# Kernel tuning notes

Measured on AMD Instinct MI355X. Metric: run time of the kernel, lower is better.

Reference implementation:

```python
import jax, jax.numpy as jnp
import numpy as np

SEED_ID = 1234  # seed_id from init, masked to 32 bits


def _synth_R(k_iter, d_out, d_in, dtype):
    # Seeded pseudo-random base weight: randn(d_out, d_in) / sqrt(d_in)
    s = (SEED_ID ^ int(k_iter)) & 0xFFFFFFFF
    R = jax.random.normal(jax.random.key(s), (d_out, d_in), dtype=dtype)
    return R * np.float32(1.0 / np.sqrt(d_in))


def setup_inputs() -> dict:
    key = jax.random.key(0)
    kx, kv, ku = jax.random.split(key, 3)
    B, S, D, RANK = 32, 4096, 512, 64
    x = jax.random.normal(kx, (B, S, D), dtype=jnp.float32)
    alpha = jnp.float32(1.0)
    U = jnp.zeros((D, RANK), dtype=jnp.float32)
    # match torch init: V ~ N(0,1)/sqrt(rank)
    V = jax.random.normal(kv, (RANK, D), dtype=jnp.float32) * np.float32(1.0 / np.sqrt(RANK))
    bias = jnp.zeros((D,), dtype=jnp.float32)
    return {"x": x, "alpha": alpha, "U": U, "V": V, "bias": bias, "k_iter": 2}


def reference(x, alpha, U, V, bias, k_iter):
    d_out = U.shape[0]
    d_in = V.shape[1]
    dtype = x.dtype
    R = _synth_R(k_iter, d_out, d_in, dtype)                      # [d_out, d_in]
    W = alpha.astype(dtype) * R + (U.astype(dtype) @ V.astype(dtype))  # [d_out, d_in]
    # F.linear: x @ W.T + b
    return jnp.einsum('bsd,od->bso', x, W) + bias.astype(dtype)
```

## Files before the change

### kernel.cpp

```cpp
#include <hip/hip_runtime.h>
#include <stdint.h>


#define M_TOTAL 131072
#define N_DIM 512
#define K_DIM 512
#define RANK 64

typedef __attribute__((ext_vector_type(8))) short bf16x8;
typedef __attribute__((ext_vector_type(4))) float f32x4;

__device__ __forceinline__ void threefry2x32(uint32_t k0, uint32_t k1,
                                             uint32_t x0, uint32_t x1,
                                             uint32_t& y0, uint32_t& y1) {
  uint32_t ks0 = k0, ks1 = k1, ks2 = k0 ^ k1 ^ 0x1BD11BDAu;
  const uint32_t ks[3] = {ks0, ks1, ks2};
  const int R0[4] = {13, 15, 26, 6};
  const int R1[4] = {17, 29, 16, 24};
  x0 += ks[0];
  x1 += ks[1];
#pragma unroll
  for (int g = 0; g < 5; ++g) {
    const int* r = (g & 1) ? R1 : R0;
#pragma unroll
    for (int i = 0; i < 4; ++i) {
      x0 += x1;
      x1 = (x1 << r[i]) | (x1 >> (32 - r[i]));
      x1 ^= x0;
    }
    x0 += ks[(g + 1) % 3];
    x1 += ks[(g + 2) % 3] + (uint32_t)(g + 1);
  }
  y0 = x0;
  y1 = x1;
}

__device__ __forceinline__ float erfinv_f32(float x) {
  float w = -log1pf(-x * x);
  float p;
  if (w < 5.0f) {
    w = w - 2.5f;
    p = 2.81022636e-08f;
    p = fmaf(p, w, 3.43273939e-07f);
    p = fmaf(p, w, -3.5233877e-06f);
    p = fmaf(p, w, -4.39150654e-06f);
    p = fmaf(p, w, 0.00021858087f);
    p = fmaf(p, w, -0.00125372503f);
    p = fmaf(p, w, -0.00417768164f);
    p = fmaf(p, w, 0.246640727f);
    p = fmaf(p, w, 1.50140941f);
  } else {
    w = sqrtf(w) - 3.0f;
    p = -0.000200214257f;
    p = fmaf(p, w, 0.000100950558f);
    p = fmaf(p, w, 0.00134934322f);
    p = fmaf(p, w, -0.00367342844f);
    p = fmaf(p, w, 0.00573950773f);
    p = fmaf(p, w, -0.0076224613f);
    p = fmaf(p, w, 0.00943887047f);
    p = fmaf(p, w, 1.00167406f);
    p = fmaf(p, w, 2.83297682f);
  }
  return p * x;
}

__device__ __forceinline__ unsigned short f32_to_bf16_rtne(float f) {
  uint32_t x = __float_as_uint(f);
  uint32_t r = (x + 0x7FFFu + ((x >> 16) & 1u)) >> 16;
  return (unsigned short)r;
}

__global__ __launch_bounds__(256) void build_w_kernel(
    const float* __restrict__ alpha_p, const float* __restrict__ U,
    const float* __restrict__ V, const int* __restrict__ k_iter_p,
    unsigned short* __restrict__ Wb) {
  int idx = blockIdx.x * blockDim.x + threadIdx.x;
  uint32_t s = (1234u ^ (uint32_t)(*k_iter_p));
  uint32_t y0, y1;
  threefry2x32(0u, s, 0u, (uint32_t)idx, y0, y1);
  uint32_t bits = y0 ^ y1;
  float u01 = __uint_as_float((bits >> 9) | 0x3f800000u) - 1.0f;
  const float lo = -0.99999994f;
  float u = fmaxf(lo, u01 * 2.0f + lo);
  float rnorm = 1.41421354f * erfinv_f32(u);
  const float scale = 0.044194173824159216f;

  int o = idx >> 9;
  int i = idx & 511;
  float uv = 0.0f;
#pragma unroll 8
  for (int r = 0; r < RANK; ++r)
    uv = fmaf(U[o * RANK + r], V[r * N_DIM + i], uv);

  float w = (*alpha_p) * (rnorm * scale) + uv;
  Wb[idx] = f32_to_bf16_rtne(w);
}

#define BM 128
#define BN 128
#define BK 64
#define LDK 72

__global__ __launch_bounds__(256, 2) void gemm_kernel(
    const float* __restrict__ X, const unsigned short* __restrict__ Wb,
    const float* __restrict__ bias, float* __restrict__ Out) {
  __shared__ unsigned short As[BM][LDK];
  __shared__ unsigned short Bs[BN][LDK];

  const int tid = threadIdx.x;
  const int bid = blockIdx.x;
  const int nb = bid & 3;
  const int mb = bid >> 2;
  const int m0 = mb * BM;
  const int n0 = nb * BN;

  const int lane = tid & 63;
  const int wave = tid >> 6;
  const int wr = wave >> 1;
  const int wc = wave & 1;

  f32x4 acc[4][4];
#pragma unroll
  for (int i = 0; i < 4; ++i)
#pragma unroll
    for (int j = 0; j < 4; ++j) acc[i][j] = (f32x4){0.f, 0.f, 0.f, 0.f};

  const int xr = tid >> 4;
  const int xc = (tid & 15) * 4;
  const int wrow = tid >> 3;
  const int wcol = (tid & 7) * 8;

  for (int kt = 0; kt < K_DIM / BK; ++kt) {
    const int k0 = kt * BK;
#pragma unroll
    for (int j = 0; j < 8; ++j) {
      int row = xr + j * 16;
      float4 v = *reinterpret_cast<const float4*>(
          &X[(size_t)(m0 + row) * K_DIM + k0 + xc]);
      ushort4 pk;
      pk.x = f32_to_bf16_rtne(v.x);
      pk.y = f32_to_bf16_rtne(v.y);
      pk.z = f32_to_bf16_rtne(v.z);
      pk.w = f32_to_bf16_rtne(v.w);
      *reinterpret_cast<ushort4*>(&As[row][xc]) = pk;
    }
#pragma unroll
    for (int j = 0; j < 4; ++j) {
      int row = wrow + j * 32;
      bf16x8 v = *reinterpret_cast<const bf16x8*>(
          &Wb[(size_t)(n0 + row) * K_DIM + k0 + wcol]);
      *reinterpret_cast<bf16x8*>(&Bs[row][wcol]) = v;
    }
    __syncthreads();

#pragma unroll
    for (int ks = 0; ks < 2; ++ks) {
      bf16x8 a[4], b[4];
#pragma unroll
      for (int i = 0; i < 4; ++i)
        a[i] = *reinterpret_cast<const bf16x8*>(
            &As[wr * 64 + i * 16 + (lane & 15)][ks * 32 + (lane >> 4) * 8]);
#pragma unroll
      for (int j = 0; j < 4; ++j)
        b[j] = *reinterpret_cast<const bf16x8*>(
            &Bs[wc * 64 + j * 16 + (lane & 15)][ks * 32 + (lane >> 4) * 8]);
#pragma unroll
      for (int i = 0; i < 4; ++i)
#pragma unroll
        for (int j = 0; j < 4; ++j)
          acc[i][j] =
              __builtin_amdgcn_mfma_f32_16x16x32_bf16(a[i], b[j], acc[i][j], 0, 0, 0);
    }
    __syncthreads();
  }

  const int col = lane & 15;
  const int rbase = (lane >> 4) * 4;
#pragma unroll
  for (int j = 0; j < 4; ++j) {
    int oc = n0 + wc * 64 + j * 16 + col;
    float bv = bias[oc];
#pragma unroll
    for (int i = 0; i < 4; ++i) {
      int orow = m0 + wr * 64 + i * 16 + rbase;
#pragma unroll
      for (int q = 0; q < 4; ++q) {
        Out[(size_t)(orow + q) * N_DIM + oc] = acc[i][j][q] + bv;
      }
    }
  }
}

extern "C" void kernel_launch(void* const* d_in, const int* in_sizes, int n_in,
                              void* d_out, int out_size, void* d_ws,
                              size_t ws_size, hipStream_t stream) {
  (void)in_sizes;
  (void)n_in;
  (void)out_size;
  (void)ws_size;
  const float* x = (const float*)d_in[0];
  const float* alpha = (const float*)d_in[1];
  const float* U = (const float*)d_in[2];
  const float* V = (const float*)d_in[3];
  const float* bias = (const float*)d_in[4];
  const int* k_iter = (const int*)d_in[5];
  float* out = (float*)d_out;
  unsigned short* Wb = (unsigned short*)d_ws;

  build_w_kernel<<<(N_DIM * K_DIM) / 256, 256, 0, stream>>>(alpha, U, V,
                                                            k_iter, Wb);
  const int grid = (M_TOTAL / BM) * (N_DIM / BN);
  gemm_kernel<<<grid, 256, 0, stream>>>(x, Wb, bias, out);
}
```

Baseline: 205.6 us.

## Prefetch next K tile into registers, packed bf16 convert, block swizzle, occupancy 3

```diff
diff --git a/kernel.cpp b/kernel.cpp
--- a/kernel.cpp
+++ b/kernel.cpp
@@ -13,8 +13,8 @@
 __device__ __forceinline__ void threefry2x32(uint32_t k0, uint32_t k1,
                                              uint32_t x0, uint32_t x1,
                                              uint32_t& y0, uint32_t& y1) {
-  uint32_t ks0 = k0, ks1 = k1, ks2 = k0 ^ k1 ^ 0x1BD11BDAu;
-  const uint32_t ks[3] = {ks0, ks1, ks2};
+  uint32_t ks2 = k0 ^ k1 ^ 0x1BD11BDAu;
+  const uint32_t ks[3] = {k0, k1, ks2};
   const int R0[4] = {13, 15, 26, 6};
   const int R1[4] = {17, 29, 16, 24};
   x0 += ks[0];
@@ -100,17 +100,19 @@
 #define BN 128
 #define BK 64
 #define LDK 72
-
-__global__ __launch_bounds__(256, 2) void gemm_kernel(
+#define NKT (K_DIM / BK)
+
+__global__ __launch_bounds__(256, 3) void gemm_kernel(
     const float* __restrict__ X, const unsigned short* __restrict__ Wb,
     const float* __restrict__ bias, float* __restrict__ Out) {
   __shared__ unsigned short As[BM][LDK];
   __shared__ unsigned short Bs[BN][LDK];
 
   const int tid = threadIdx.x;
-  const int bid = blockIdx.x;
-  const int nb = bid & 3;
-  const int mb = bid >> 2;
+  const int p = blockIdx.x;
+  const int l = (p & 7) * 512 + (p >> 3);
+  const int nb = l & 3;
+  const int mb = l >> 2;
   const int m0 = mb * BM;
   const int n0 = nb * BN;
 
@@ -130,28 +132,48 @@
   const int wrow = tid >> 3;
   const int wcol = (tid & 7) * 8;
 
-  for (int kt = 0; kt < K_DIM / BK; ++kt) {
-    const int k0 = kt * BK;
-#pragma unroll
-    for (int j = 0; j < 8; ++j) {
-      int row = xr + j * 16;
-      float4 v = *reinterpret_cast<const float4*>(
-          &X[(size_t)(m0 + row) * K_DIM + k0 + xc]);
-      ushort4 pk;
-      pk.x = f32_to_bf16_rtne(v.x);
-      pk.y = f32_to_bf16_rtne(v.y);
-      pk.z = f32_to_bf16_rtne(v.z);
-      pk.w = f32_to_bf16_rtne(v.w);
-      *reinterpret_cast<ushort4*>(&As[row][xc]) = pk;
-    }
-#pragma unroll
-    for (int j = 0; j < 4; ++j) {
-      int row = wrow + j * 32;
-      bf16x8 v = *reinterpret_cast<const bf16x8*>(
-          &Wb[(size_t)(n0 + row) * K_DIM + k0 + wcol]);
-      *reinterpret_cast<bf16x8*>(&Bs[row][wcol]) = v;
-    }
-    __syncthreads();
+  float4 xv[8];
+  bf16x8 wv[4];
+
+#define ISSUE_LOADS(kt_)                                                   \
+  {                                                                        \
+    const int k0_ = (kt_)*BK;                                              \
+    _Pragma("unroll") for (int j = 0; j < 8; ++j) xv[j] =                  \
+        *reinterpret_cast<const float4*>(                                  \
+            &X[(size_t)(m0 + xr + j * 16) * K_DIM + k0_ + xc]);            \
+    _Pragma("unroll") for (int j = 0; j < 4; ++j) wv[j] =                  \
+        *reinterpret_cast<const bf16x8*>(                                  \
+            &Wb[(size_t)(n0 + wrow + j * 32) * K_DIM + k0_ + wcol]);       \
+  }
+
+#define WRITE_LDS()                                                        \
+  {                                                                        \
+    _Pragma("unroll") for (int j = 0; j < 8; ++j) {                        \
+      uint32_t p0_, p1_;                                                   \
+      asm("v_cvt_pk_bf16_f32 %0, %1, %2"                                   \
+          : "=v"(p0_)                                                      \
+          : "v"(xv[j].x), "v"(xv[j].y));                                   \
+      asm("v_cvt_pk_bf16_f32 %0, %1, %2"                                   \
+          : "=v"(p1_)                                                      \
+          : "v"(xv[j].z), "v"(xv[j].w));                                   \
+      uint2 pk_;                                                           \
+      pk_.x = p0_;                                                         \
+      pk_.y = p1_;                                                         \
+      *reinterpret_cast<uint2*>(&As[xr + j * 16][xc]) = pk_;               \
+    }                                                                      \
+    _Pragma("unroll") for (int j = 0; j < 4; ++j)                          \
+        *reinterpret_cast<bf16x8*>(&Bs[wrow + j * 32][wcol]) = wv[j];      \
+  }
+
+  ISSUE_LOADS(0)
+  WRITE_LDS()
+  __syncthreads();
+
+  for (int kt = 0; kt < NKT; ++kt) {
+    if (kt < NKT - 1) {
+      ISSUE_LOADS(kt + 1)
+      asm volatile("" ::: "memory");
+    }
 
 #pragma unroll
     for (int ks = 0; ks < 2; ++ks) {
@@ -168,10 +190,15 @@
       for (int i = 0; i < 4; ++i)
 #pragma unroll
         for (int j = 0; j < 4; ++j)
-          acc[i][j] =
-              __builtin_amdgcn_mfma_f32_16x16x32_bf16(a[i], b[j], acc[i][j], 0, 0, 0);
+          acc[i][j] = __builtin_amdgcn_mfma_f32_16x16x32_bf16(a[i], b[j],
+                                                              acc[i][j], 0, 0, 0);
     }
     __syncthreads();
+
+    if (kt < NKT - 1) {
+      WRITE_LDS()
+      __syncthreads();
+    }
   }
 
   const int col = lane & 15;
@@ -189,6 +216,8 @@
       }
     }
   }
+#undef ISSUE_LOADS
+#undef WRITE_LDS
 }
 
 extern "C" void kernel_launch(void* const* d_in, const int* in_sizes, int n_in,
```

After: 165.0 us. -19.7%, faster.

## Keep full W slice resident in LDS and stream X directly into registers

Applied to the files above, without the earlier changes.

```diff
diff --git a/kernel.cpp b/kernel.cpp
--- a/kernel.cpp
+++ b/kernel.cpp
@@ -7,14 +7,21 @@
 #define K_DIM 512
 #define RANK 64
 
+#define BN_BLK 128
+#define BM_TILE 128
+#define MT_PER_BLK 8
+#define LDW 520
+#define NSTEP 16
+#define PF 4
+
 typedef __attribute__((ext_vector_type(8))) short bf16x8;
 typedef __attribute__((ext_vector_type(4))) float f32x4;
 
 __device__ __forceinline__ void threefry2x32(uint32_t k0, uint32_t k1,
                                              uint32_t x0, uint32_t x1,
                                              uint32_t& y0, uint32_t& y1) {
-  uint32_t ks0 = k0, ks1 = k1, ks2 = k0 ^ k1 ^ 0x1BD11BDAu;
-  const uint32_t ks[3] = {ks0, ks1, ks2};
+  uint32_t ks2 = k0 ^ k1 ^ 0x1BD11BDAu;
+  const uint32_t ks[3] = {k0, k1, ks2};
   const int R0[4] = {13, 15, 26, 6};
   const int R1[4] = {17, 29, 16, 24};
   x0 += ks[0];
@@ -96,98 +103,126 @@
   Wb[idx] = f32_to_bf16_rtne(w);
 }
 
-#define BM 128
-#define BN 128
-#define BK 64
-#define LDK 72
-
-__global__ __launch_bounds__(256, 2) void gemm_kernel(
+__device__ __forceinline__ bf16x8 cvt8(const float4& lo, const float4& hi) {
+  union {
+    bf16x8 v;
+    uint32_t d[4];
+  } au;
+  asm("v_cvt_pk_bf16_f32 %0, %1, %2" : "=v"(au.d[0]) : "v"(lo.x), "v"(lo.y));
+  asm("v_cvt_pk_bf16_f32 %0, %1, %2" : "=v"(au.d[1]) : "v"(lo.z), "v"(lo.w));
+  asm("v_cvt_pk_bf16_f32 %0, %1, %2" : "=v"(au.d[2]) : "v"(hi.x), "v"(hi.y));
+  asm("v_cvt_pk_bf16_f32 %0, %1, %2" : "=v"(au.d[3]) : "v"(hi.z), "v"(hi.w));
+  return au.v;
+}
+
+__global__ __launch_bounds__(512, 2) void gemm_kernel(
     const float* __restrict__ X, const unsigned short* __restrict__ Wb,
     const float* __restrict__ bias, float* __restrict__ Out) {
-  __shared__ unsigned short As[BM][LDK];
-  __shared__ unsigned short Bs[BN][LDK];
+  extern __shared__ unsigned short Ws[];
 
   const int tid = threadIdx.x;
-  const int bid = blockIdx.x;
-  const int nb = bid & 3;
-  const int mb = bid >> 2;
-  const int m0 = mb * BM;
-  const int n0 = nb * BN;
+  const int p = blockIdx.x;
+  const int l = (p & 7) * 64 + (p >> 3);
+  const int nb = l & 3;
+  const int mg = l >> 2;
+  const int n0 = nb * BN_BLK;
+  const size_t blk_m = (size_t)mg * (BM_TILE * MT_PER_BLK);
+
+#pragma unroll
+  for (int it = 0; it < 16; ++it) {
+    int u = it * 512 + tid;
+    int row = u >> 6;
+    int c = u & 63;
+    bf16x8 v = *reinterpret_cast<const bf16x8*>(
+        &Wb[(size_t)(n0 + row) * K_DIM + c * 8]);
+    *reinterpret_cast<bf16x8*>(&Ws[row * LDW + c * 8]) = v;
+  }
+  __syncthreads();
 
   const int lane = tid & 63;
   const int wave = tid >> 6;
-  const int wr = wave >> 1;
-  const int wc = wave & 1;
-
-  f32x4 acc[4][4];
-#pragma unroll
-  for (int i = 0; i < 4; ++i)
-#pragma unroll
-    for (int j = 0; j < 4; ++j) acc[i][j] = (f32x4){0.f, 0.f, 0.f, 0.f};
-
-  const int xr = tid >> 4;
-  const int xc = (tid & 15) * 4;
-  const int wrow = tid >> 3;
-  const int wcol = (tid & 7) * 8;
-
-  for (int kt = 0; kt < K_DIM / BK; ++kt) {
-    const int k0 = kt * BK;
-#pragma unroll
-    for (int j = 0; j < 8; ++j) {
-      int row = xr + j * 16;
-      float4 v = *reinterpret_cast<const float4*>(
-          &X[(size_t)(m0 + row) * K_DIM + k0 + xc]);
-      ushort4 pk;
-      pk.x = f32_to_bf16_rtne(v.x);
-      pk.y = f32_to_bf16_rtne(v.y);
-      pk.z = f32_to_bf16_rtne(v.z);
-      pk.w = f32_to_bf16_rtne(v.w);
-      *reinterpret_cast<ushort4*>(&As[row][xc]) = pk;
-    }
-#pragma unroll
-    for (int j = 0; j < 4; ++j) {
-      int row = wrow + j * 32;
-      bf16x8 v = *reinterpret_cast<const bf16x8*>(
-          &Wb[(size_t)(n0 + row) * K_DIM + k0 + wcol]);
-      *reinterpret_cast<bf16x8*>(&Bs[row][wcol]) = v;
-    }
-    __syncthreads();
-
-#pragma unroll
-    for (int ks = 0; ks < 2; ++ks) {
-      bf16x8 a[4], b[4];
-#pragma unroll
-      for (int i = 0; i < 4; ++i)
-        a[i] = *reinterpret_cast<const bf16x8*>(
-            &As[wr * 64 + i * 16 + (lane & 15)][ks * 32 + (lane >> 4) * 8]);
-#pragma unroll
-      for (int j = 0; j < 4; ++j)
-        b[j] = *reinterpret_cast<const bf16x8*>(
-            &Bs[wc * 64 + j * 16 + (lane & 15)][ks * 32 + (lane >> 4) * 8]);
-#pragma unroll
-      for (int i = 0; i < 4; ++i)
-#pragma unroll
-        for (int j = 0; j < 4; ++j)
-          acc[i][j] =
-              __builtin_amdgcn_mfma_f32_16x16x32_bf16(a[i], b[j], acc[i][j], 0, 0, 0);
-    }
-    __syncthreads();
-  }
-
-  const int col = lane & 15;
-  const int rbase = (lane >> 4) * 4;
-#pragma unroll
-  for (int j = 0; j < 4; ++j) {
-    int oc = n0 + wc * 64 + j * 16 + col;
-    float bv = bias[oc];
+  const int wm = wave >> 2;
+  const int wn = wave & 3;
+  const int r = lane & 15;
+  const int g = lane >> 4;
+
+  const float* xbase = X + (blk_m + wm * 64 + r) * K_DIM + g * 8;
+  const int wsbase = (wn * 32 + r) * LDW + g * 8;
+
+  float bv[2];
+#pragma unroll
+  for (int jj = 0; jj < 2; ++jj)
+    bv[jj] = bias[n0 + wn * 32 + jj * 16 + r];
+
+  float4 xq[PF][4][2];
+
+  const float* xm = xbase;
+#pragma unroll
+  for (int s = 0; s < PF; ++s)
 #pragma unroll
     for (int i = 0; i < 4; ++i) {
-      int orow = m0 + wr * 64 + i * 16 + rbase;
-#pragma unroll
-      for (int q = 0; q < 4; ++q) {
-        Out[(size_t)(orow + q) * N_DIM + oc] = acc[i][j][q] + bv;
+      xq[s][i][0] = *reinterpret_cast<const float4*>(xm + (size_t)i * 16 * K_DIM + s * 32);
+      xq[s][i][1] = *reinterpret_cast<const float4*>(xm + (size_t)i * 16 * K_DIM + s * 32 + 4);
+    }
+
+  for (int mt = 0; mt < MT_PER_BLK; ++mt) {
+    f32x4 acc[4][2];
+#pragma unroll
+    for (int i = 0; i < 4; ++i)
+#pragma unroll
+      for (int jj = 0; jj < 2; ++jj) acc[i][jj] = (f32x4){0.f, 0.f, 0.f, 0.f};
+
+#pragma unroll
+    for (int s = 0; s < NSTEP; ++s) {
+      const int slot = s % PF;
+      bf16x8 a[4];
+#pragma unroll
+      for (int i = 0; i < 4; ++i) a[i] = cvt8(xq[slot][i][0], xq[slot][i][1]);
+
+      if (s < NSTEP - PF) {
+#pragma unroll
+        for (int i = 0; i < 4; ++i) {
+          xq[slot][i][0] = *reinterpret_cast<const float4*>(
+              xm + (size_t)i * 16 * K_DIM + (s + PF) * 32);
+          xq[slot][i][1] = *reinterpret_cast<const float4*>(
+              xm + (size_t)i * 16 * K_DIM + (s + PF) * 32 + 4);
+        }
+      } else if (mt < MT_PER_BLK - 1) {
+        const float* xn = xm + (size_t)BM_TILE * K_DIM;
+#pragma unroll
+        for (int i = 0; i < 4; ++i) {
+          xq[slot][i][0] = *reinterpret_cast<const float4*>(
+              xn + (size_t)i * 16 * K_DIM + (s + PF - NSTEP) * 32);
+          xq[slot][i][1] = *reinterpret_cast<const float4*>(
+              xn + (size_t)i * 16 * K_DIM + (s + PF - NSTEP) * 32 + 4);
+        }
       }
-    }
+
+#pragma unroll
+      for (int jj = 0; jj < 2; ++jj) {
+        bf16x8 b = *reinterpret_cast<const bf16x8*>(
+            &Ws[wsbase + jj * 16 * LDW + s * 32]);
+#pragma unroll
+        for (int i = 0; i < 4; ++i)
+          acc[i][jj] = __builtin_amdgcn_mfma_f32_16x16x32_bf16(a[i], b,
+                                                               acc[i][jj], 0, 0, 0);
+      }
+    }
+
+    const size_t mrow0 = blk_m + (size_t)mt * BM_TILE + wm * 64 + (lane >> 4) * 4;
+#pragma unroll
+    for (int jj = 0; jj < 2; ++jj) {
+      const int oc = n0 + wn * 32 + jj * 16 + r;
+#pragma unroll
+      for (int i = 0; i < 4; ++i) {
+        const size_t rb = mrow0 + i * 16;
+#pragma unroll
+        for (int q = 0; q < 4; ++q)
+          Out[(rb + q) * N_DIM + oc] = acc[i][jj][q] + bv[jj];
+      }
+    }
+
+    xm += (size_t)BM_TILE * K_DIM;
   }
 }
 
@@ -209,6 +244,10 @@
 
   build_w_kernel<<<(N_DIM * K_DIM) / 256, 256, 0, stream>>>(alpha, U, V,
                                                             k_iter, Wb);
-  const int grid = (M_TOTAL / BM) * (N_DIM / BN);
-  gemm_kernel<<<grid, 256, 0, stream>>>(x, Wb, bias, out);
-}
+
+  const int lds_bytes = BN_BLK * LDW * 2;
+  hipFuncSetAttribute((const void*)gemm_kernel,
+                      hipFuncAttributeMaxDynamicSharedMemorySize, lds_bytes);
+  const int grid = 4 * (M_TOTAL / (BM_TILE * MT_PER_BLK));
+  gemm_kernel<<<grid, 512, lds_bytes, stream>>>(x, Wb, bias, out);
+}
```

Result: slower. 491.6 us (+139.1%).
